# Performance work log

Hardware: AMD Instinct MI355X
Metric: run time of the kernel (lower is better)

The kernel has to match this reference:

```python
import jax, jax.numpy as jnp
import numpy as np

B, L, C, O, K, KN, A = 32, 4096, 256, 256, 3, 4, 16
BN_EPS = 1e-5


def setup_inputs() -> dict:
    key = jax.random.key(0)
    ks = jax.random.split(key, 12)
    x = jax.random.normal(ks[0], (B, L, C), dtype=jnp.float32)
    # ODConv weight bank [kernel_num, out, in//groups, k], kaiming-ish scale
    weight = jax.random.normal(ks[1], (KN, O, C, K), dtype=jnp.float32) * np.sqrt(2.0 / (O * K))
    w_fc = jax.random.normal(ks[2], (A, C), dtype=jnp.float32) * np.sqrt(2.0 / A)
    bn_gamma = jnp.ones((A,), jnp.float32)
    bn_beta = jnp.zeros((A,), jnp.float32)
    bn_mean = jnp.zeros((A,), jnp.float32)
    bn_var = jnp.ones((A,), jnp.float32)
    w_ch = jax.random.normal(ks[3], (C, A), dtype=jnp.float32) * np.sqrt(2.0 / C)
    b_ch = jnp.zeros((C,), jnp.float32)
    w_fil = jax.random.normal(ks[4], (O, A), dtype=jnp.float32) * np.sqrt(2.0 / O)
    b_fil = jnp.zeros((O,), jnp.float32)
    w_sp = jax.random.normal(ks[5], (K, A), dtype=jnp.float32) * np.sqrt(2.0 / K)
    b_sp = jnp.zeros((K,), jnp.float32)
    w_ker = jax.random.normal(ks[6], (KN, A), dtype=jnp.float32) * np.sqrt(2.0 / KN)
    b_ker = jnp.zeros((KN,), jnp.float32)
    return {"x": x, "weight": weight, "w_fc": w_fc, "bn_gamma": bn_gamma,
            "bn_beta": bn_beta, "bn_mean": bn_mean, "bn_var": bn_var,
            "w_ch": w_ch, "b_ch": b_ch, "w_fil": w_fil, "b_fil": b_fil,
            "w_sp": w_sp, "b_sp": b_sp, "w_ker": w_ker, "b_ker": b_ker}


def reference(x, weight, w_fc, bn_gamma, bn_beta, bn_mean, bn_var,
              w_ch, b_ch, w_fil, b_fil, w_sp, b_sp, w_ker, b_ker):
    # x: [B, L, C] channels-last; attention head uses global-avg-pooled features
    pooled = x.mean(axis=1)                                   # [B, C]
    h = pooled @ w_fc.T                                       # [B, A] (1x1 conv, no bias)
    h = (h - bn_mean) * jax.lax.rsqrt(bn_var + BN_EPS) * bn_gamma + bn_beta
    h = jax.nn.relu(h)
    # temperature = 1.0
    ch_att = jax.nn.sigmoid(h @ w_ch.T + b_ch)                # [B, C]  channel attention
    fil_att = jax.nn.sigmoid(h @ w_fil.T + b_fil)             # [B, O]  filter attention
    sp_att = jax.nn.sigmoid(h @ w_sp.T + b_sp)                # [B, K]  spatial attention
    ker_att = jax.nn.softmax(h @ w_ker.T + b_ker, axis=1)     # [B, KN] kernel attention
    # aggregate per-sample dynamic kernel: [B, O, C, K]
    agg_w = jnp.einsum('bk,bn,noik->boik', sp_att, ker_att, weight)
    xs = x.transpose(0, 2, 1) * ch_att[:, :, None]            # [B, C, L]

    def conv1(xi, wi):  # xi: [C, L], wi: [O, C, K]
        return jax.lax.conv_general_dilated(
            xi[None], wi, window_strides=(1,), padding=[(1, 1)],
            rhs_dilation=(1,), dimension_numbers=('NCH', 'OIH', 'NCH'))[0]

    out = jax.vmap(conv1)(xs, agg_w)                          # [B, O, L]
    return out * fil_att[:, :, None]
```

## Files before the change

### kernel.cpp

```cpp
#include <hip/hip_runtime.h>
#include <hip/hip_bf16.h>
#include <stdint.h>

#define B_ 32
#define L_ 4096
#define C_ 256
#define O_ 256
#define K_ 3
#define KN_ 4
#define A_ 16
#define LP_ 4098

typedef unsigned short u16;
typedef __attribute__((ext_vector_type(8))) short bf16x8;
typedef __attribute__((ext_vector_type(4))) float f32x4;

#define GLDS16(gp, lp_) __builtin_amdgcn_global_load_lds( \
    (const __attribute__((address_space(1))) void*)(gp),  \
    (__attribute__((address_space(3))) void*)(lp_), 16, 0, 0)

static __device__ __forceinline__ u16 f2bf(float f) {
    union { float f; uint32_t u; } v; v.f = f;
    uint32_t u = v.u;
    u += 0x7fffu + ((u >> 16) & 1u);
    return (u16)(u >> 16);
}

__global__ __launch_bounds__(256) void poolcvt_k(const float* __restrict__ x,
                                                 u16* __restrict__ xb,
                                                 float* __restrict__ part) {
    __shared__ float red[4][256];
    int bid = blockIdx.x;
    int b = bid >> 5, chunk = bid & 31;
    int t = threadIdx.x;
    int w = t >> 6, lane = t & 63;
    int c0 = lane << 2;
    int h = lane >> 5;
    int grp = (lane & 31) >> 1;
    int sub = lane & 1;
    f32x4 s = {0.f, 0.f, 0.f, 0.f};
    const float* xp = x + ((size_t)b * L_ + (size_t)chunk * 128) * C_ + c0;
    u16* xbb = xb + ((size_t)b * LP_ + (size_t)chunk * 128 + 1) * 256;
    #pragma unroll 4
    for (int it = 0; it < 32; ++it) {
        int rl = it * 4 + w;
        int l = chunk * 128 + rl;
        float4 v = *reinterpret_cast<const float4*>(xp + (size_t)rl * C_);
        s.x += v.x; s.y += v.y; s.z += v.z; s.w += v.w;
        ushort4 hv;
        hv.x = f2bf(v.x); hv.y = f2bf(v.y); hv.z = f2bf(v.z); hv.w = f2bf(v.w);
        int slot = grp ^ ((l + 1) & 7);
        *reinterpret_cast<ushort4*>(xbb + (size_t)rl * 256 + h * 128 + slot * 8 + sub * 4) = hv;
    }
    *reinterpret_cast<f32x4*>(&red[w][c0]) = s;
    __syncthreads();
    part[((size_t)bid << 8) + t] = red[0][t] + red[1][t] + red[2][t] + red[3][t];
    if (chunk == 0 && t < 64)
        *reinterpret_cast<ushort4*>(xb + (size_t)b * LP_ * 256 + t * 4) = make_ushort4(0, 0, 0, 0);
    if (chunk == 31 && t < 64)
        *reinterpret_cast<ushort4*>(xb + ((size_t)b * LP_ + LP_ - 1) * 256 + t * 4) = make_ushort4(0, 0, 0, 0);
}

__global__ __launch_bounds__(256) void pool_partial_k(const float* __restrict__ x,
                                                      float* __restrict__ part) {
    int bid = blockIdx.x;
    int b = bid >> 5, ch = bid & 31;
    int c = threadIdx.x;
    const float* p = x + (size_t)(b * L_ + ch * 128) * C_ + c;
    float s = 0.f;
    #pragma unroll 4
    for (int l = 0; l < 128; ++l) s += p[(size_t)l * C_];
    part[((size_t)bid << 8) + c] = s;
}

__global__ __launch_bounds__(256) void att_k(const float* __restrict__ part,
    const float* __restrict__ w_fc, const float* __restrict__ bn_g,
    const float* __restrict__ bn_b, const float* __restrict__ bn_m,
    const float* __restrict__ bn_v,
    const float* __restrict__ w_ch, const float* __restrict__ b_ch,
    const float* __restrict__ w_fil, const float* __restrict__ b_fil,
    const float* __restrict__ w_sp, const float* __restrict__ b_sp,
    const float* __restrict__ w_ker, const float* __restrict__ b_ker,
    float* __restrict__ ch_att, float* __restrict__ fil_att,
    float* __restrict__ sp_att, float* __restrict__ ker_att) {
    __shared__ float pooled[C_];
    __shared__ float h[A_];
    int b = blockIdx.x, t = threadIdx.x;
    float s = 0.f;
    for (int j = 0; j < 32; ++j) s += part[(((size_t)(b * 32 + j)) << 8) + t];
    pooled[t] = s * (1.0f / L_);
    __syncthreads();
    if (t < A_) {
        float acc = 0.f;
        for (int c = 0; c < C_; ++c) acc += pooled[c] * w_fc[t * C_ + c];
        float sc = bn_g[t] * rsqrtf(bn_v[t] + 1e-5f);
        acc = (acc - bn_m[t]) * sc + bn_b[t];
        h[t] = fmaxf(acc, 0.f);
    }
    __syncthreads();
    {
        float a1 = b_ch[t], a2 = b_fil[t];
        for (int a = 0; a < A_; ++a) { a1 += h[a] * w_ch[t * A_ + a]; a2 += h[a] * w_fil[t * A_ + a]; }
        ch_att[b * C_ + t]  = 1.f / (1.f + expf(-a1));
        fil_att[b * O_ + t] = 1.f / (1.f + expf(-a2));
    }
    if (t < K_) {
        float acc = b_sp[t];
        for (int a = 0; a < A_; ++a) acc += h[a] * w_sp[t * A_ + a];
        sp_att[b * 4 + t] = 1.f / (1.f + expf(-acc));
    }
    if (t == 0) {
        float lg[KN_], m = -1e30f;
        for (int n = 0; n < KN_; ++n) {
            float acc = b_ker[n];
            for (int a = 0; a < A_; ++a) acc += h[a] * w_ker[n * A_ + a];
            lg[n] = acc; m = fmaxf(m, acc);
        }
        float ss = 0.f;
        for (int n = 0; n < KN_; ++n) { lg[n] = expf(lg[n] - m); ss += lg[n]; }
        for (int n = 0; n < KN_; ++n) ker_att[b * 4 + n] = lg[n] / ss;
    }
}

__global__ __launch_bounds__(256) void wfrag_k(const float* __restrict__ weight,
    const float* __restrict__ ch_att, const float* __restrict__ fil_att,
    const float* __restrict__ sp_att, const float* __restrict__ ker_att,
    u16* __restrict__ wf) {
    __shared__ float wlds[64 * 97];
    int beta = blockIdx.x;
    int ob = beta & 15, ic = (beta >> 4) & 7, bg = beta >> 7;
    int t = threadIdx.x;
    const size_t blk_base = (size_t)(ob * 16) * 768 + ic * 96;
    #pragma unroll
    for (int j = 0; j < 24; ++j) {
        int ei = t + (j << 8);
        int r = ei / 96, c = ei - r * 96;
        int n = r >> 4, ol = r & 15;
        wlds[r * 97 + c] = weight[((size_t)n * 256 + ol) * 768 + blk_base + c];
    }
    __syncthreads();
    int lane = t & 63, q = t >> 6;
    int o_l = lane & 15, ig = lane >> 4;
    int i0 = ig << 3;
    int o = (ob << 4) + o_l;
    int ig0 = (ic << 5) + i0;
    float wl[4][3][8];
    #pragma unroll
    for (int n = 0; n < 4; ++n) {
        int rb = (n * 16 + o_l) * 97;
        #pragma unroll
        for (int e = 0; e < 8; ++e) {
            int cb = rb + (i0 + e) * 3;
            wl[n][0][e] = wlds[cb];
            wl[n][1][e] = wlds[cb + 1];
            wl[n][2][e] = wlds[cb + 2];
        }
    }
    #pragma unroll
    for (int bi = 0; bi < 2; ++bi) {
        int b = (bg << 3) + (q << 1) + bi;
        float ka0 = ker_att[b * 4 + 0], ka1 = ker_att[b * 4 + 1];
        float ka2 = ker_att[b * 4 + 2], ka3 = ker_att[b * 4 + 3];
        float fil = fil_att[b * O_ + o];
        float ch8[8];
        *reinterpret_cast<float4*>(ch8)     = *reinterpret_cast<const float4*>(ch_att + b * C_ + ig0);
        *reinterpret_cast<float4*>(ch8 + 4) = *reinterpret_cast<const float4*>(ch_att + b * C_ + ig0 + 4);
        #pragma unroll
        for (int tap = 0; tap < 3; ++tap) {
            float fs = fil * sp_att[b * 4 + tap];
            union { u16 h[8]; uint4 v; } pk;
            #pragma unroll
            for (int e = 0; e < 8; ++e) {
                float acc = ka0 * wl[0][tap][e] + ka1 * wl[1][tap][e]
                          + ka2 * wl[2][tap][e] + ka3 * wl[3][tap][e];
                pk.h[e] = f2bf(acc * fs * ch8[e]);
            }
            size_t idx = ((((size_t)(b * 24 + tap * 8 + ic) * 16 + ob) * 64) + lane) << 3;
            *reinterpret_cast<uint4*>(wf + idx) = pk.v;
        }
    }
}

__global__ __launch_bounds__(512, 4) void conv_k(const u16* __restrict__ xb,
    const u16* __restrict__ wf, float* __restrict__ out) {
    __shared__ uint4 lds4[4224];
    char* lp = (char*)lds4;
    int phys = blockIdx.x;
    int logical = ((phys & 7) << 7) + (phys >> 3);
    int b = logical >> 5, lb = logical & 31;
    int l0 = lb << 7;
    int tid = threadIdx.x;
    int w = tid >> 6, lane = tid & 63;
    int wr = w & 3, wc = w >> 2;
    int lrow = lane & 15;
    int g = lane >> 4;

    const u16* xrow = xb + ((size_t)b * LP_ + l0) * 256;

    auto stage_half = [&](int h, int bufoff) {
        const u16* gb = xrow + h * 128;
        #pragma unroll
        for (int j = 0; j < 4; ++j) {
            const u16* ga = gb + (size_t)(w * 16 + j * 4 + (lane >> 4)) * 256 + (lane & 15) * 8;
            GLDS16(ga, lp + bufoff + w * 4096 + j * 1024);
        }
        if (w == 0) {
            const u16* ga = gb + (size_t)(128 + ((lane >> 4) & 1)) * 256 + (lane & 15) * 8;
            GLDS16(ga, lp + bufoff + 32768);
        }
    };

    f32x4 acc[4][4] = {};

    auto compute_half = [&](int h, int bufoff) {
        for (int kk = 0; kk < 12; ++kk) {
            int tap = kk >> 2, ich = kk & 3;
            int kc = tap * 8 + h * 4 + ich;
            bf16x8 af[4], bfr[4];
            const u16* wp = wf + ((((size_t)(b * 24 + kc) * 16 + wr * 4) * 64 + lane) << 3);
            #pragma unroll
            for (int m = 0; m < 4; ++m)
                af[m] = *reinterpret_cast<const bf16x8*>(wp + (m << 9));
            int slotbase = (ich << 2) + g;
            #pragma unroll
            for (int n = 0; n < 4; ++n) {
                int row = wc * 64 + n * 16 + lrow + tap;
                int off = bufoff + row * 256 + (((slotbase ^ (row & 7))) << 4);
                bfr[n] = *reinterpret_cast<const bf16x8*>(lp + off);
            }
            #pragma unroll
            for (int m = 0; m < 4; ++m)
                #pragma unroll
                for (int n = 0; n < 4; ++n)
                    acc[m][n] = __builtin_amdgcn_mfma_f32_16x16x32_bf16(af[m], bfr[n], acc[m][n], 0, 0, 0);
        }
    };

    stage_half(0, 0);
    __syncthreads();
    stage_half(1, 33792);
    compute_half(0, 0);
    __syncthreads();
    compute_half(1, 33792);
    __syncthreads();

    float* ep = (float*)(lp + w * 8192);
    size_t obase = (size_t)b * O_ * L_;
    int lcol = l0 + wc * 64;
    #pragma unroll
    for (int c2 = 0; c2 < 2; ++c2) {
        #pragma unroll
        for (int m2 = 0; m2 < 2; ++m2) {
            int m = c2 * 2 + m2;
            #pragma unroll
            for (int n = 0; n < 4; ++n) {
                int l_loc = n * 16 + lrow;
                int sl = (l_loc >> 2);
                #pragma unroll
                for (int j = 0; j < 4; ++j) {
                    int o_loc = m2 * 16 + g * 4 + j;
                    ep[o_loc * 64 + ((sl ^ o_loc) & 15) * 4 + (l_loc & 3)] = acc[m][n][j];
                }
            }
        }
        #pragma unroll
        for (int og = 0; og < 8; ++og) {
            int o_loc = og * 4 + g;
            int l4 = lrow;
            float4 v = *reinterpret_cast<float4*>(ep + o_loc * 64 + ((l4 ^ o_loc) & 15) * 4);
            int o = wr * 64 + c2 * 32 + o_loc;
            *reinterpret_cast<float4*>(out + obase + (size_t)o * L_ + lcol + l4 * 4) = v;
        }
        if (c2 == 0) __syncthreads();
    }
}

__global__ __launch_bounds__(512, 4) void conv_fb_k(const float* __restrict__ x,
    const u16* __restrict__ wf, float* __restrict__ out) {
    __shared__ uint4 lds4[4160];
    char* lp = (char*)lds4;
    int phys = blockIdx.x;
    int logical = ((phys & 7) << 7) + (phys >> 3);
    int b = logical >> 5, lb = logical & 31;
    int l0 = lb << 7;
    int tid = threadIdx.x;
    const size_t xbase = (size_t)b * L_ * C_;
    #pragma unroll 4
    for (int it = 0; it < 17; ++it) {
        int id = tid + (it << 9);
        if (id < 8320) {
            int r  = id >> 6;
            int i  = (id & 63) << 2;
            int lg = l0 - 1 + r;
            float4 v = make_float4(0.f, 0.f, 0.f, 0.f);
            if (lg >= 0 && lg < L_)
                v = *reinterpret_cast<const float4*>(x + xbase + (size_t)lg * C_ + i);
            ushort4 hv;
            hv.x = f2bf(v.x); hv.y = f2bf(v.y); hv.z = f2bf(v.z); hv.w = f2bf(v.w);
            int slot = (i >> 3) ^ (r & 7);
            int off = r * 512 + slot * 16 + ((i >> 2) & 1) * 8;
            *reinterpret_cast<ushort4*>(lp + off) = hv;
        }
    }
    __syncthreads();
    int w = tid >> 6, lane = tid & 63;
    int wr = w & 3, wc = w >> 2;
    int lrow = lane & 15;
    int g = lane >> 4;
    f32x4 acc[4][4] = {};
    for (int kc = 0; kc < 24; ++kc) {
        int t  = kc >> 3;
        int ic = kc & 7;
        bf16x8 af[4], bfr[4];
        const u16* wp = wf + ((((size_t)(b * 24 + kc) * 16 + wr * 4) * 64 + lane) << 3);
        #pragma unroll
        for (int m = 0; m < 4; ++m)
            af[m] = *reinterpret_cast<const bf16x8*>(wp + (m << 9));
        int slotbase = (ic << 2) + g;
        #pragma unroll
        for (int n = 0; n < 4; ++n) {
            int row = wc * 64 + n * 16 + lrow + t;
            int off = row * 512 + ((slotbase ^ (row & 7)) << 4);
            bfr[n] = *reinterpret_cast<const bf16x8*>(lp + off);
        }
        #pragma unroll
        for (int m = 0; m < 4; ++m)
            #pragma unroll
            for (int n = 0; n < 4; ++n)
                acc[m][n] = __builtin_amdgcn_mfma_f32_16x16x32_bf16(af[m], bfr[n], acc[m][n], 0, 0, 0);
    }
    __syncthreads();
    float* ep = (float*)(lp + w * 8192);
    size_t obase = (size_t)b * O_ * L_;
    int lcol = l0 + wc * 64;
    #pragma unroll
    for (int c2 = 0; c2 < 2; ++c2) {
        #pragma unroll
        for (int m2 = 0; m2 < 2; ++m2) {
            int m = c2 * 2 + m2;
            #pragma unroll
            for (int n = 0; n < 4; ++n) {
                int l_loc = n * 16 + lrow;
                int sl = (l_loc >> 2);
                #pragma unroll
                for (int j = 0; j < 4; ++j) {
                    int o_loc = m2 * 16 + g * 4 + j;
                    ep[o_loc * 64 + ((sl ^ o_loc) & 15) * 4 + (l_loc & 3)] = acc[m][n][j];
                }
            }
        }
        #pragma unroll
        for (int og = 0; og < 8; ++og) {
            int o_loc = og * 4 + g;
            int l4 = lrow;
            float4 v = *reinterpret_cast<float4*>(ep + o_loc * 64 + ((l4 ^ o_loc) & 15) * 4);
            int o = wr * 64 + c2 * 32 + o_loc;
            *reinterpret_cast<float4*>(out + obase + (size_t)o * L_ + lcol + l4 * 4) = v;
        }
        if (c2 == 0) __syncthreads();
    }
}

extern "C" void kernel_launch(void* const* d_in, const int* in_sizes, int n_in,
                              void* d_out, int out_size, void* d_ws, size_t ws_size,
                              hipStream_t stream) {
    const float* x      = (const float*)d_in[0];
    const float* weight = (const float*)d_in[1];
    const float* w_fc   = (const float*)d_in[2];
    const float* bn_g   = (const float*)d_in[3];
    const float* bn_b   = (const float*)d_in[4];
    const float* bn_m   = (const float*)d_in[5];
    const float* bn_v   = (const float*)d_in[6];
    const float* w_ch   = (const float*)d_in[7];
    const float* b_ch   = (const float*)d_in[8];
    const float* w_fil  = (const float*)d_in[9];
    const float* b_fil  = (const float*)d_in[10];
    const float* w_sp   = (const float*)d_in[11];
    const float* b_sp   = (const float*)d_in[12];
    const float* w_ker  = (const float*)d_in[13];
    const float* b_ker  = (const float*)d_in[14];
    float* out = (float*)d_out;
    char*  ws  = (char*)d_ws;

    float* part    = (float*)ws;
    float* ch_att  = (float*)(ws + (1 << 20));
    float* fil_att = ch_att + 32 * 256;
    float* sp_att  = fil_att + 32 * 256;
    float* ker_att = sp_att + 32 * 4;
    u16*   wfrag   = (u16*)(ws + (1 << 20) + 70 * 1024);
    u16*   xbf     = (u16*)(ws + (16u << 20));
    const size_t need = (16u << 20) + (size_t)B_ * LP_ * 512;

    if (ws_size >= need) {
        poolcvt_k<<<1024, 256, 0, stream>>>(x, xbf, part);
        att_k<<<32, 256, 0, stream>>>(part, w_fc, bn_g, bn_b, bn_m, bn_v,
                                      w_ch, b_ch, w_fil, b_fil, w_sp, b_sp, w_ker, b_ker,
                                      ch_att, fil_att, sp_att, ker_att);
        wfrag_k<<<512, 256, 0, stream>>>(weight, ch_att, fil_att, sp_att, ker_att, wfrag);
        conv_k<<<1024, 512, 0, stream>>>(xbf, wfrag, out);
    } else {
        pool_partial_k<<<1024, 256, 0, stream>>>(x, part);
        att_k<<<32, 256, 0, stream>>>(part, w_fc, bn_g, bn_b, bn_m, bn_v,
                                      w_ch, b_ch, w_fil, b_fil, w_sp, b_sp, w_ker, b_ker,
                                      ch_att, fil_att, sp_att, ker_att);
        wfrag_k<<<512, 256, 0, stream>>>(weight, ch_att, fil_att, sp_att, ker_att, wfrag);
        conv_fb_k<<<1024, 512, 0, stream>>>(x, wfrag, out);
    }
}
```

Baseline: 120.4 us.

## Stage full input tile with register loads and drop half-split async LDS pipeline

The conversion kernel now writes bf16 activations in plain channel order instead of a pre-swizzled layout. The conv kernel loads the whole 130-row tile into LDS with ordinary vector loads, applies the XOR swizzle on the LDS store, and then runs one 24-step MFMA loop. This replaces the two-half global_load_lds staging, which overlapped loading the second half with computing the first. The new path is simpler and needs only one barrier before compute, but it gives up that load/compute overlap and routes staging through registers.

```diff
diff --git a/kernel.cpp b/kernel.cpp
--- a/kernel.cpp
+++ b/kernel.cpp
@@ -14,10 +14,6 @@
 typedef unsigned short u16;
 typedef __attribute__((ext_vector_type(8))) short bf16x8;
 typedef __attribute__((ext_vector_type(4))) float f32x4;
-
-#define GLDS16(gp, lp_) __builtin_amdgcn_global_load_lds( \
-    (const __attribute__((address_space(1))) void*)(gp),  \
-    (__attribute__((address_space(3))) void*)(lp_), 16, 0, 0)
 
 static __device__ __forceinline__ u16 f2bf(float f) {
     union { float f; uint32_t u; } v; v.f = f;
@@ -35,22 +31,17 @@
     int t = threadIdx.x;
     int w = t >> 6, lane = t & 63;
     int c0 = lane << 2;
-    int h = lane >> 5;
-    int grp = (lane & 31) >> 1;
-    int sub = lane & 1;
     f32x4 s = {0.f, 0.f, 0.f, 0.f};
     const float* xp = x + ((size_t)b * L_ + (size_t)chunk * 128) * C_ + c0;
     u16* xbb = xb + ((size_t)b * LP_ + (size_t)chunk * 128 + 1) * 256;
     #pragma unroll 4
     for (int it = 0; it < 32; ++it) {
         int rl = it * 4 + w;
-        int l = chunk * 128 + rl;
         float4 v = *reinterpret_cast<const float4*>(xp + (size_t)rl * C_);
         s.x += v.x; s.y += v.y; s.z += v.z; s.w += v.w;
         ushort4 hv;
         hv.x = f2bf(v.x); hv.y = f2bf(v.y); hv.z = f2bf(v.z); hv.w = f2bf(v.w);
-        int slot = grp ^ ((l + 1) & 7);
-        *reinterpret_cast<ushort4*>(xbb + (size_t)rl * 256 + h * 128 + slot * 8 + sub * 4) = hv;
+        *reinterpret_cast<ushort4*>(xbb + (size_t)rl * 256 + c0) = hv;
     }
     *reinterpret_cast<f32x4*>(&red[w][c0]) = s;
     __syncthreads();
@@ -183,65 +174,55 @@
 
 __global__ __launch_bounds__(512, 4) void conv_k(const u16* __restrict__ xb,
     const u16* __restrict__ wf, float* __restrict__ out) {
-    __shared__ uint4 lds4[4224];
+    __shared__ uint4 lds4[4160];
     char* lp = (char*)lds4;
     int phys = blockIdx.x;
     int logical = ((phys & 7) << 7) + (phys >> 3);
     int b = logical >> 5, lb = logical & 31;
     int l0 = lb << 7;
     int tid = threadIdx.x;
+    const u16* xbb = xb + (size_t)b * LP_ * 256;
+
+    #pragma unroll
+    for (int it = 0; it < 9; ++it) {
+        int id = tid + (it << 9);
+        if (id < 4160) {
+            int r = id >> 5, g16 = id & 31;
+            bf16x8 v = *reinterpret_cast<const bf16x8*>(xbb + ((size_t)(l0 + r) << 8) + g16 * 8);
+            *reinterpret_cast<bf16x8*>(lp + r * 512 + ((g16 ^ (r & 7)) << 4)) = v;
+        }
+    }
+    __syncthreads();
+
     int w = tid >> 6, lane = tid & 63;
     int wr = w & 3, wc = w >> 2;
     int lrow = lane & 15;
     int g = lane >> 4;
 
-    const u16* xrow = xb + ((size_t)b * LP_ + l0) * 256;
-
-    auto stage_half = [&](int h, int bufoff) {
-        const u16* gb = xrow + h * 128;
-        #pragma unroll
-        for (int j = 0; j < 4; ++j) {
-            const u16* ga = gb + (size_t)(w * 16 + j * 4 + (lane >> 4)) * 256 + (lane & 15) * 8;
-            GLDS16(ga, lp + bufoff + w * 4096 + j * 1024);
-        }
-        if (w == 0) {
-            const u16* ga = gb + (size_t)(128 + ((lane >> 4) & 1)) * 256 + (lane & 15) * 8;
-            GLDS16(ga, lp + bufoff + 32768);
-        }
-    };
-
     f32x4 acc[4][4] = {};
 
-    auto compute_half = [&](int h, int bufoff) {
-        for (int kk = 0; kk < 12; ++kk) {
-            int tap = kk >> 2, ich = kk & 3;
-            int kc = tap * 8 + h * 4 + ich;
-            bf16x8 af[4], bfr[4];
-            const u16* wp = wf + ((((size_t)(b * 24 + kc) * 16 + wr * 4) * 64 + lane) << 3);
-            #pragma unroll
-            for (int m = 0; m < 4; ++m)
-                af[m] = *reinterpret_cast<const bf16x8*>(wp + (m << 9));
-            int slotbase = (ich << 2) + g;
-            #pragma unroll
-            for (int n = 0; n < 4; ++n) {
-                int row = wc * 64 + n * 16 + lrow + tap;
-                int off = bufoff + row * 256 + (((slotbase ^ (row & 7))) << 4);
-                bfr[n] = *reinterpret_cast<const bf16x8*>(lp + off);
-            }
-            #pragma unroll
-            for (int m = 0; m < 4; ++m)
-                #pragma unroll
-                for (int n = 0; n < 4; ++n)
-                    acc[m][n] = __builtin_amdgcn_mfma_f32_16x16x32_bf16(af[m], bfr[n], acc[m][n], 0, 0, 0);
-        }
-    };
-
-    stage_half(0, 0);
-    __syncthreads();
-    stage_half(1, 33792);
-    compute_half(0, 0);
-    __syncthreads();
-    compute_half(1, 33792);
+    for (int kc = 0; kc < 24; ++kc) {
+        int t  = kc >> 3;
+        int ic = kc & 7;
+        bf16x8 af[4], bfr[4];
+        const u16* wp = wf + ((((size_t)(b * 24 + kc) * 16 + wr * 4) * 64 + lane) << 3);
+        #pragma unroll
+        for (int m = 0; m < 4; ++m)
+            af[m] = *reinterpret_cast<const bf16x8*>(wp + (m << 9));
+        int slotbase = (ic << 2) + g;
+        #pragma unroll
+        for (int n = 0; n < 4; ++n) {
+            int row = wc * 64 + n * 16 + lrow + t;
+            int off = row * 512 + ((slotbase ^ (row & 7)) << 4);
+            bfr[n] = *reinterpret_cast<const bf16x8*>(lp + off);
+        }
+        #pragma unroll
+        for (int m = 0; m < 4; ++m)
+            #pragma unroll
+            for (int n = 0; n < 4; ++n)
+                acc[m][n] = __builtin_amdgcn_mfma_f32_16x16x32_bf16(af[m], bfr[n], acc[m][n], 0, 0, 0);
+    }
+
     __syncthreads();
 
     float* ep = (float*)(lp + w * 8192);
```

Result: no change. 120.4 us (+0.0%).
